# Kernel tuning notes

Measured on AMD Instinct MI355X. Metric: run time of the kernel, lower is better.

## Reference

```python
import jax, jax.numpy as jnp
import numpy as np

NUM_GROUPS = 32
RANK = 64            # per-head rank (uniform)
IN_FEATURES = 4096
OUT_FEATURES = 4096
GROUP_DIM = OUT_FEATURES // NUM_GROUPS  # 128
SUM_RANKS = NUM_GROUPS * RANK           # 2048


def setup_inputs() -> dict:
    key = jax.random.key(0)
    k1, k2, k3 = jax.random.split(key, 3)
    hidden_states = jax.random.normal(k1, (4, 4096, IN_FEATURES), dtype=jnp.float32)
    # VT: nn.Linear(in_features, sum(ranks), bias=False) -> weight [sum_ranks, in]
    VT_weight = jax.random.normal(k2, (SUM_RANKS, IN_FEATURES), dtype=jnp.float32) * (1.0 / np.sqrt(IN_FEATURES))
    # U_list: per-group nn.Linear(r, group_dim), init.normal_ -> stacked [G, group_dim, r]
    U_weight = jax.random.normal(k3, (NUM_GROUPS, GROUP_DIM, RANK), dtype=jnp.float32)
    return {"hidden_states": hidden_states, "VT_weight": VT_weight, "U_weight": U_weight}


def reference(hidden_states, VT_weight, U_weight):
    # shared down-projection: [B,S,in] @ [in,sum_ranks] -> [B,S,sum_ranks]
    z = jnp.einsum('bsi,ri->bsr', hidden_states, VT_weight)
    B, S, _ = z.shape
    # grouped up-projection (block-diagonal GEMM): slice per group -> [B,S,G,r]
    zg = z.reshape(B, S, NUM_GROUPS, RANK)
    out = jnp.einsum('bsgr,gdr->bsgd', zg, U_weight)  # [B,S,G,group_dim]
    return out.reshape(B, S, NUM_GROUPS * GROUP_DIM)  # concat along last dim
```

## Files before the change

### kernel.cpp

```cpp
#include <hip/hip_runtime.h>
#include <hip/hip_bf16.h>
#include <stdint.h>

typedef __attribute__((ext_vector_type(8)))  short bf16x8;
typedef __attribute__((ext_vector_type(4)))  float f32x4;
typedef __attribute__((ext_vector_type(4)))  float float4v;
typedef __attribute__((ext_vector_type(8)))  unsigned short u16x8;

#define MFMA16(a,b,c) __builtin_amdgcn_mfma_f32_16x16x32_bf16((a),(b),(c),0,0,0)

__device__ __forceinline__ unsigned short f2bf(float f) {
    unsigned int u = __builtin_bit_cast(unsigned int, f);
    u = (u + 0x7fffu + ((u >> 16) & 1u)) >> 16;
    return (unsigned short)u;
}

__device__ __forceinline__ void gload_lds16(const void* g, void* l) {
    __builtin_amdgcn_global_load_lds(
        (const __attribute__((address_space(1))) void*)g,
        (__attribute__((address_space(3))) void*)l, 16, 0, 0);
}

template<int N> __device__ __forceinline__ void waitvm() {}
template<> __device__ __forceinline__ void waitvm<6>() { asm volatile("s_waitcnt vmcnt(6)" ::: "memory"); }
template<> __device__ __forceinline__ void waitvm<4>() { asm volatile("s_waitcnt vmcnt(4)" ::: "memory"); }
template<> __device__ __forceinline__ void waitvm<2>() { asm volatile("s_waitcnt vmcnt(2)" ::: "memory"); }
template<> __device__ __forceinline__ void waitvm<0>() { asm volatile("s_waitcnt vmcnt(0)" ::: "memory"); }

__global__ void cvt_f32_bf16(const float* __restrict__ in, unsigned short* __restrict__ out, long n) {
    long i = ((long)blockIdx.x * blockDim.x + threadIdx.x) * 8;
    long stride = (long)gridDim.x * blockDim.x * 8;
    for (; i < n; i += stride) {
        float4v v0 = *(const float4v*)(in + i);
        float4v v1 = *(const float4v*)(in + i + 4);
        u16x8 o;
        o[0] = f2bf(v0[0]); o[1] = f2bf(v0[1]); o[2] = f2bf(v0[2]); o[3] = f2bf(v0[3]);
        o[4] = f2bf(v1[0]); o[5] = f2bf(v1[1]); o[6] = f2bf(v1[2]); o[7] = f2bf(v1[3]);
        *(u16x8*)(out + i) = o;
    }
}


#define STAGE_A(nA_, k0n, h, l) \
    gload_lds16(pA + ((l)*128 + (h)*64) * 4096L + (k0n), (nA_) + dA0 + ((l)*128 + (h)*64) * 64)
#define STAGE_B(nB_, k0n, h, l) \
    gload_lds16(pB + ((l)*128 + (h)*32) * 4096L + (k0n), (nB_) + dB0 + ((l)*128 + (h)*32) * 64)

#define LDA(sA_, QM) do { _Pragma("unroll") for (int mi = 0; mi < 4; ++mi) { \
    a[mi][0] = *(const bf16x8*)((sA_) + ((wr*128 + (QM)*64 + mi*16 + lan15) << 6) + g0); \
    a[mi][1] = *(const bf16x8*)((sA_) + ((wr*128 + (QM)*64 + mi*16 + lan15) << 6) + (g0 ^ 32)); } } while (0)
#define LDB(dst_, sB_, QN) do { _Pragma("unroll") for (int ni = 0; ni < 2; ++ni) { \
    dst_[ni][0] = *(const bf16x8*)((sB_) + ((wc*64 + (QN)*32 + ni*16 + lan15) << 6) + g0); \
    dst_[ni][1] = *(const bf16x8*)((sB_) + ((wc*64 + (QN)*32 + ni*16 + lan15) << 6) + (g0 ^ 32)); } } while (0)

#define DOMFMA(QM, QN, bset_) do { __builtin_amdgcn_s_setprio(1); \
    _Pragma("unroll") for (int mi = 0; mi < 4; ++mi) \
      _Pragma("unroll") for (int ni = 0; ni < 2; ++ni) { \
        acc[(QM)*4+mi][(QN)*2+ni] = MFMA16(a[mi][0], bset_[ni][0], acc[(QM)*4+mi][(QN)*2+ni]); \
        acc[(QM)*4+mi][(QN)*2+ni] = MFMA16(a[mi][1], bset_[ni][1], acc[(QM)*4+mi][(QN)*2+ni]); } \
    __builtin_amdgcn_s_setprio(0); } while (0)

#define BAR1() do { __builtin_amdgcn_s_barrier(); \
    asm volatile("s_waitcnt lgkmcnt(0)" ::: "memory"); \
    __builtin_amdgcn_sched_barrier(0); } while (0)
#define BAR2() do { __builtin_amdgcn_s_barrier(); \
    __builtin_amdgcn_sched_barrier(0); } while (0)

#define KTILE(sA_, sB_, nA_, nB_, k0n, DOSTAGE, V0, V1, V3) do { \
     \
    LDA(sA_, 0); LDB(b0, sB_, 0); \
    if (DOSTAGE) { STAGE_A(nA_, k0n, 0, 0); STAGE_A(nA_, k0n, 0, 1); \
                   STAGE_B(nB_, k0n, 0, 0); STAGE_B(nB_, k0n, 0, 1); } \
    BAR1(); DOMFMA(0, 0, b0); waitvm<V0>(); BAR2(); \
     \
    LDB(b1, sB_, 1); \
    if (DOSTAGE) { STAGE_B(nB_, k0n, 1, 0); STAGE_B(nB_, k0n, 1, 1); } \
    BAR1(); DOMFMA(0, 1, b1); waitvm<V1>(); BAR2(); \
     \
    LDA(sA_, 1); \
    if (DOSTAGE) { STAGE_A(nA_, k0n, 1, 0); STAGE_A(nA_, k0n, 1, 1); } \
    BAR1(); DOMFMA(1, 1, b1); BAR2(); \
     \
    BAR1(); DOMFMA(1, 0, b0); waitvm<V3>(); BAR2(); \
} while (0)

__global__ __launch_bounds__(512, 2) void gemm1_8ph(const unsigned short* __restrict__ A,
                                                    const unsigned short* __restrict__ B,
                                                    unsigned short* __restrict__ Z) {
    __shared__ __align__(16) unsigned short lds[65536];

    const int tid   = threadIdx.x;
    const int lane  = tid & 63;
    const int wid   = tid >> 6;
    const int wr    = wid >> 2;
    const int wc    = wid & 3;
    const int lan15 = lane & 15;
    const int g0    = (((lane >> 4) ^ (lane & 7)) << 3);

    const int  bid = blockIdx.x;
    const long m0  = (long)(bid >> 3) * 256;
    const long n0  = (long)(bid & 7) * 256;

    const int q8    = tid >> 3;
    const int granA = (((tid & 7) ^ (q8 & 7)) << 3);
    const unsigned short* pA = A + (m0 + q8) * 4096L + granA;
    const int rB0   = (q8 & 31) + ((q8 >> 5) << 6);
    const unsigned short* pB = B + (n0 + rB0) * 4096L + granA;
    const int dA0   = (wid * 8) * 64;
    const int dB0   = ((wid & 3) * 8 + ((wid >> 2) << 6)) * 64;

    f32x4 acc[8][4] = {};
    bf16x8 a[4][2], b0[2][2], b1[2][2];

    unsigned short* buf0 = lds;
    unsigned short* buf1 = lds + 32768;

    STAGE_A(buf0, 0, 0, 0); STAGE_A(buf0, 0, 0, 1);
    STAGE_B(buf0 + 16384, 0, 0, 0); STAGE_B(buf0 + 16384, 0, 0, 1);
    STAGE_B(buf0 + 16384, 0, 1, 0); STAGE_B(buf0 + 16384, 0, 1, 1);
    STAGE_A(buf0, 0, 1, 0); STAGE_A(buf0, 0, 1, 1);
    waitvm<4>();
    BAR2();

    for (int t = 0; t < 63; ++t) {
        unsigned short* cb = (t & 1) ? buf1 : buf0;
        unsigned short* nb = (t & 1) ? buf0 : buf1;
        KTILE(cb, cb + 16384, nb, nb + 16384, (t + 1) * 64, true, 6, 6, 4);
    }
    KTILE(buf1, buf1 + 16384, buf0, buf0 + 16384, 0, false, 2, 0, -1);

    const int rq = (lane >> 4) << 2;
    #pragma unroll
    for (int mi = 0; mi < 8; ++mi) {
        #pragma unroll
        for (int ni = 0; ni < 4; ++ni) {
            const long mb  = m0 + wr * 128 + mi * 16 + rq;
            const long nb2 = n0 + wc * 64 + ni * 16 + lan15;
            #pragma unroll
            for (int j = 0; j < 4; ++j)
                Z[(mb + j) * 2048L + nb2] = f2bf(acc[mi][ni][j]);
        }
    }
}

#define U_PAD 80

__global__ __launch_bounds__(256) void gemm2(const unsigned short* __restrict__ Z,
                                             const float* __restrict__ U,
                                             float* __restrict__ out) {
    __shared__ __align__(16) unsigned short lU[128 * U_PAD];

    const int tid  = threadIdx.x;
    const int lane = tid & 63;
    const int wid  = tid >> 6;
    const int g    = blockIdx.x & 31;
    const long m0  = (long)(blockIdx.x >> 5) * 64;

    const float* ug = U + (long)g * (128 * 64);
    for (int i = tid; i < (128 * 64) / 4; i += 256) {
        const int r = i >> 4;
        const int c = (i << 2) & 63;
        float4v v = *(const float4v*)(ug + i * 4);
        unsigned short* d = &lU[r * U_PAD + c];
        d[0] = f2bf(v[0]); d[1] = f2bf(v[1]); d[2] = f2bf(v[2]); d[3] = f2bf(v[3]);
    }
    __syncthreads();

    const long mrow = m0 + wid * 16 + (lane & 15);
    const unsigned short* zrow = Z + mrow * 2048L + g * 64 + ((lane >> 4) << 3);
    const bf16x8 a0 = *(const bf16x8*)(zrow);
    const bf16x8 a1 = *(const bf16x8*)(zrow + 32);

    f32x4 acc[8] = {};
    const int blds = (lane & 15);
    const int kofs = (lane >> 4) << 3;
    #pragma unroll
    for (int ni = 0; ni < 8; ++ni) {
        const bf16x8 c0 = *(const bf16x8*)&lU[(ni * 16 + blds) * U_PAD + kofs];
        const bf16x8 c1 = *(const bf16x8*)&lU[(ni * 16 + blds) * U_PAD + 32 + kofs];
        acc[ni] = MFMA16(a0, c0, acc[ni]);
        acc[ni] = MFMA16(a1, c1, acc[ni]);
    }

    const long mb = m0 + wid * 16 + ((lane >> 4) << 2);
    const long cb = (long)g * 128 + (lane & 15);
    #pragma unroll
    for (int ni = 0; ni < 8; ++ni)
        #pragma unroll
        for (int j = 0; j < 4; ++j)
            out[(mb + j) * 4096L + cb + ni * 16] = acc[ni][j];
}

extern "C" void kernel_launch(void* const* d_in, const int* in_sizes, int n_in,
                              void* d_out, int out_size, void* d_ws, size_t ws_size,
                              hipStream_t stream) {
    const float* hs = (const float*)d_in[0];
    const float* vt = (const float*)d_in[1];
    const float* uw = (const float*)d_in[2];
    float* out = (float*)d_out;

    unsigned short* hs_bf = (unsigned short*)d_ws;
    unsigned short* vt_bf = hs_bf + 67108864L;
    unsigned short* z_bf  = vt_bf + 8388608L;

    cvt_f32_bf16<<<2048, 256, 0, stream>>>(hs, hs_bf, 67108864L);
    cvt_f32_bf16<<<512, 256, 0, stream>>>(vt, vt_bf, 8388608L);

    gemm1_8ph<<<512, 512, 0, stream>>>(hs_bf, vt_bf, z_bf);

    gemm2<<<8192, 256, 0, stream>>>(z_bf, uw, out);
}
```

Baseline: 373.5 us.

## Restructure GEMM1 main loop into two-tile staggered prefetch pipeline

The first GEMM's K loop is rewritten to process two K tiles per iteration with fixed A/B buffer pointers. Global-to-LDS loads for upcoming tiles are spread across all eight MFMA phases and issued further ahead, instead of two-phase double buffering with wait points in every phase. Fewer vmcnt waits and a deeper prefetch distance should keep the MFMA units fed and remove the per-iteration buffer pointer selection. The tighter overlap of LDS writes with LDS reads of the same buffer makes the barrier and wait counts more delicate, which risks races or stalls if the counts are off.

```diff
diff --git a/kernel.cpp b/kernel.cpp
--- a/kernel.cpp
+++ b/kernel.cpp
@@ -23,8 +23,6 @@
 
 template<int N> __device__ __forceinline__ void waitvm() {}
 template<> __device__ __forceinline__ void waitvm<6>() { asm volatile("s_waitcnt vmcnt(6)" ::: "memory"); }
-template<> __device__ __forceinline__ void waitvm<4>() { asm volatile("s_waitcnt vmcnt(4)" ::: "memory"); }
-template<> __device__ __forceinline__ void waitvm<2>() { asm volatile("s_waitcnt vmcnt(2)" ::: "memory"); }
 template<> __device__ __forceinline__ void waitvm<0>() { asm volatile("s_waitcnt vmcnt(0)" ::: "memory"); }
 
 __global__ void cvt_f32_bf16(const float* __restrict__ in, unsigned short* __restrict__ out, long n) {
@@ -66,22 +64,29 @@
 #define BAR2() do { __builtin_amdgcn_s_barrier(); \
     __builtin_amdgcn_sched_barrier(0); } while (0)
 
-#define KTILE(sA_, sB_, nA_, nB_, k0n, DOSTAGE, V0, V1, V3) do { \
-     \
-    LDA(sA_, 0); LDB(b0, sB_, 0); \
-    if (DOSTAGE) { STAGE_A(nA_, k0n, 0, 0); STAGE_A(nA_, k0n, 0, 1); \
-                   STAGE_B(nB_, k0n, 0, 0); STAGE_B(nB_, k0n, 0, 1); } \
-    BAR1(); DOMFMA(0, 0, b0); waitvm<V0>(); BAR2(); \
-     \
-    LDB(b1, sB_, 1); \
-    if (DOSTAGE) { STAGE_B(nB_, k0n, 1, 0); STAGE_B(nB_, k0n, 1, 1); } \
-    BAR1(); DOMFMA(0, 1, b1); waitvm<V1>(); BAR2(); \
-     \
-    LDA(sA_, 1); \
-    if (DOSTAGE) { STAGE_A(nA_, k0n, 1, 0); STAGE_A(nA_, k0n, 1, 1); } \
-    BAR1(); DOMFMA(1, 1, b1); BAR2(); \
-     \
-    BAR1(); DOMFMA(1, 0, b0); waitvm<V3>(); BAR2(); \
+#define ITER8(K1, K2, K3, S2, S3, V4, V8) do { \
+   LDA(bA0, 0); LDB(b0, bB0, 0); \
+         STAGE_A(bA1, K1, 1, 0); STAGE_A(bA1, K1, 1, 1); \
+         BAR1(); DOMFMA(0, 0, b0); BAR2(); \
+   LDB(b1, bB0, 1); \
+         if (S2) { STAGE_A(bA0, K2, 0, 0); STAGE_A(bA0, K2, 0, 1); } \
+         BAR1(); DOMFMA(0, 1, b1); BAR2(); \
+   LDA(bA0, 1); \
+         if (S2) { STAGE_B(bB0, K2, 0, 0); STAGE_B(bB0, K2, 0, 1); } \
+         BAR1(); DOMFMA(1, 1, b1); BAR2(); \
+   if (S2) { STAGE_B(bB0, K2, 1, 0); STAGE_B(bB0, K2, 1, 1); } \
+         BAR1(); DOMFMA(1, 0, b0); waitvm<V4>(); BAR2(); \
+   LDA(bA1, 0); LDB(b0, bB1, 0); \
+         if (S2) { STAGE_A(bA0, K2, 1, 0); STAGE_A(bA0, K2, 1, 1); } \
+         BAR1(); DOMFMA(0, 0, b0); BAR2(); \
+   LDB(b1, bB1, 1); \
+         if (S3) { STAGE_A(bA1, K3, 0, 0); STAGE_A(bA1, K3, 0, 1); } \
+         BAR1(); DOMFMA(0, 1, b1); BAR2(); \
+   LDA(bA1, 1); \
+         if (S3) { STAGE_B(bB1, K3, 0, 0); STAGE_B(bB1, K3, 0, 1); } \
+         BAR1(); DOMFMA(1, 1, b1); BAR2(); \
+   if (S3) { STAGE_B(bB1, K3, 1, 0); STAGE_B(bB1, K3, 1, 1); } \
+         BAR1(); DOMFMA(1, 0, b0); waitvm<V8>(); BAR2(); \
 } while (0)
 
 __global__ __launch_bounds__(512, 2) void gemm1_8ph(const unsigned short* __restrict__ A,
@@ -112,22 +117,25 @@
     f32x4 acc[8][4] = {};
     bf16x8 a[4][2], b0[2][2], b1[2][2];
 
-    unsigned short* buf0 = lds;
-    unsigned short* buf1 = lds + 32768;
-
-    STAGE_A(buf0, 0, 0, 0); STAGE_A(buf0, 0, 0, 1);
-    STAGE_B(buf0 + 16384, 0, 0, 0); STAGE_B(buf0 + 16384, 0, 0, 1);
-    STAGE_B(buf0 + 16384, 0, 1, 0); STAGE_B(buf0 + 16384, 0, 1, 1);
-    STAGE_A(buf0, 0, 1, 0); STAGE_A(buf0, 0, 1, 1);
-    waitvm<4>();
+    unsigned short* bA0 = lds;
+    unsigned short* bB0 = lds + 16384;
+    unsigned short* bA1 = lds + 32768;
+    unsigned short* bB1 = lds + 49152;
+
+    STAGE_A(bA0, 0, 0, 0);  STAGE_A(bA0, 0, 0, 1);
+    STAGE_B(bB0, 0, 0, 0);  STAGE_B(bB0, 0, 0, 1);
+    STAGE_B(bB0, 0, 1, 0);  STAGE_B(bB0, 0, 1, 1);
+    STAGE_A(bA0, 0, 1, 0);  STAGE_A(bA0, 0, 1, 1);
+    STAGE_A(bA1, 64, 0, 0); STAGE_A(bA1, 64, 0, 1);
+    STAGE_B(bB1, 64, 0, 0); STAGE_B(bB1, 64, 0, 1);
+    STAGE_B(bB1, 64, 1, 0); STAGE_B(bB1, 64, 1, 1);
+    waitvm<6>();
     BAR2();
 
-    for (int t = 0; t < 63; ++t) {
-        unsigned short* cb = (t & 1) ? buf1 : buf0;
-        unsigned short* nb = (t & 1) ? buf0 : buf1;
-        KTILE(cb, cb + 16384, nb, nb + 16384, (t + 1) * 64, true, 6, 6, 4);
-    }
-    KTILE(buf1, buf1 + 16384, buf0, buf0 + 16384, 0, false, 2, 0, -1);
+    for (int i = 0; i < 31; ++i) {
+        ITER8((2 * i + 1) * 64, (2 * i + 2) * 64, (2 * i + 3) * 64, true, true, 6, 6);
+    }
+    ITER8(63 * 64, 0, 0, false, false, 0, -1);
 
     const int rq = (lane >> 4) << 2;
     #pragma unroll
```

Measured after the change: 364.0 us. 2.5% less time.
